# Optimization experiments

Measured on AMD Instinct MI355X. Metric: run time of the kernel, lower is better.

The kernel has to match this reference:

```python
import jax, jax.numpy as jnp
import numpy as np
from jax import lax

FEAT_STRIDE = 16
SCALES = np.array([8, 16, 32], dtype=np.float64)
RATIOS = np.array([0.5, 1, 2], dtype=np.float64)
PRE_NMS_TOP_N = 6000
POST_NMS_TOP_N = 1000
NMS_THRESH = 0.7

# ---- anchor generation (numpy, static constants) ----

def _whctrs(a):
    w = a[2] - a[0] + 1.0
    h = a[3] - a[1] + 1.0
    return w, h, a[0] + 0.5 * (w - 1.0), a[1] + 0.5 * (h - 1.0)

def _mkanchors(ws, hs, xc, yc):
    return np.stack([xc - 0.5 * (ws - 1.0), yc - 0.5 * (hs - 1.0),
                     xc + 0.5 * (ws - 1.0), yc + 0.5 * (hs - 1.0)], axis=1)

def _ratio_enum(anchor, ratios):
    w, h, xc, yc = _whctrs(anchor)
    size = w * h
    ws = np.round(np.sqrt(size / ratios))
    hs = np.round(ws * ratios)
    return _mkanchors(ws, hs, xc, yc)

def _scale_enum(anchor, scales):
    w, h, xc, yc = _whctrs(anchor)
    return _mkanchors(w * scales, h * scales, xc, yc)

def generate_anchors(base_size=16):
    base = np.array([1, 1, base_size, base_size], dtype=np.float64) - 1.0
    ra = _ratio_enum(base, RATIOS)
    return np.vstack([_scale_enum(ra[i], SCALES) for i in range(ra.shape[0])]).astype(np.float32)


def setup_inputs() -> dict:
    key = jax.random.key(0)
    k1, k2 = jax.random.split(key)
    H, W, A = 76, 128, 9
    scores = jax.random.uniform(k1, (1, 2 * A, H, W), dtype=jnp.float32)
    bbox_delta = jax.random.normal(k2, (1, 4 * A, H, W), dtype=jnp.float32) * 0.1
    im_info = jnp.array([H * FEAT_STRIDE, W * FEAT_STRIDE, 1.0], dtype=jnp.float32)  # [h, w, scale]
    return {"scores": scores, "bbox_delta": bbox_delta, "im_info": im_info}


def reference(scores, bbox_delta, im_info):
    anchors = generate_anchors()            # [A, 4]
    A = anchors.shape[0]
    H, W = scores.shape[2], scores.shape[3]

    # grid of shifted anchors: [K*A, 4], anchor index varies fastest (matches permute layout)
    sx = np.arange(W) * FEAT_STRIDE
    sy = np.arange(H) * FEAT_STRIDE
    sx, sy = np.meshgrid(sx, sy)
    shifts = np.stack([sx.ravel(), sy.ravel(), sx.ravel(), sy.ravel()], axis=1).astype(np.float32)  # [K,4]
    all_anchors = jnp.asarray((anchors[None, :, :] + shifts[:, None, :]).reshape(-1, 4))  # [K*A,4]

    # foreground scores, NHWC flatten -> [K*A]
    fg = jnp.transpose(scores[0, A:], (1, 2, 0)).reshape(-1)
    # deltas, NHWC flatten -> [K*A, 4]
    deltas = jnp.transpose(bbox_delta[0], (1, 2, 0)).reshape(-1, 4)

    aw = all_anchors[:, 2] - all_anchors[:, 0] + 1.0
    ah = all_anchors[:, 3] - all_anchors[:, 1] + 1.0
    acx = all_anchors[:, 0] + 0.5 * aw
    acy = all_anchors[:, 1] + 0.5 * ah
    pcx = deltas[:, 0] * aw + acx
    pcy = deltas[:, 1] * ah + acy
    pw = jnp.exp(deltas[:, 2]) * aw
    ph = jnp.exp(deltas[:, 3]) * ah
    boxes = jnp.stack([pcx - 0.5 * pw, pcy - 0.5 * ph, pcx + 0.5 * pw, pcy + 0.5 * ph], axis=1)

    # clip_boxes to image
    xmax = im_info[1] - 1.0
    ymax = im_info[0] - 1.0
    boxes = jnp.stack([jnp.clip(boxes[:, 0], 0.0, xmax), jnp.clip(boxes[:, 1], 0.0, ymax),
                       jnp.clip(boxes[:, 2], 0.0, xmax), jnp.clip(boxes[:, 3], 0.0, ymax)], axis=1)

    # pre-NMS top-N by fg score
    top_scores, top_idx = lax.top_k(fg, PRE_NMS_TOP_N)
    props = boxes[top_idx]                  # [N, 4], sorted by score desc

    # pairwise IoU (+1 convention)
    x1, y1, x2, y2 = props[:, 0], props[:, 1], props[:, 2], props[:, 3]
    areas = (x2 - x1 + 1.0) * (y2 - y1 + 1.0)
    iw = jnp.clip(jnp.minimum(x2[:, None], x2[None, :]) - jnp.maximum(x1[:, None], x1[None, :]) + 1.0, 0.0)
    ih = jnp.clip(jnp.minimum(y2[:, None], y2[None, :]) - jnp.maximum(y1[:, None], y1[None, :]) + 1.0, 0.0)
    inter = iw * ih
    iou = inter / (areas[:, None] + areas[None, :] - inter)  # [N, N]

    # sequential greedy NMS over score-sorted boxes
    N = PRE_NMS_TOP_N
    later = jnp.arange(N)
    def body(i, keep):
        sup = (iou[i] > NMS_THRESH) & keep[i] & (later > i)
        return keep & ~sup
    keep = lax.fori_loop(0, N, body, jnp.ones((N,), dtype=bool))

    masked = jnp.where(keep, top_scores, -jnp.inf)
    _, sel = lax.top_k(masked, POST_NMS_TOP_N)
    return props[sel]                       # [POST_NMS_TOP_N, 4]
```

## Files before the change

### kernel.cpp

```cpp
#include <hip/hip_runtime.h>
#include <cstdint>

#define HH 76
#define WW 128
#define AA 9
#define HWH (HH * WW)
#define KK (HWH * AA)
#define NSEL 6000
#define NCH 94
#define NPAD (NCH * 64)
#define NOUT 1000
#define NMS_T 0.7
#define NTRI (NCH * (NCH + 1) / 2)
#define MASK_BLOCKS 1117
#define SELCAP 16384
#define BINCAP 2048
#define HIST_BLOCKS 22
#define NBIN 16384

#define LBAR() asm volatile("s_waitcnt lgkmcnt(0)\n\ts_barrier" ::: "memory")

#define WS_HIST 0
#define WS_BINB 65536
#define WS_NACT 65540
#define WS_DONE1 65544
#define WS_ZERO_BYTES 65552
#define WS_ACTIVE 65552
#define WS_BINBASE 98320
#define WS_SELKEYS 163856
#define WS_BOXES 294928
#define WS_MASK 391184

__device__ __constant__ float c_ax1[9] = {-84.f, -176.f, -360.f, -56.f, -120.f, -248.f, -36.f, -80.f, -168.f};
__device__ __constant__ float c_ay1[9] = {-40.f, -88.f, -184.f, -56.f, -120.f, -248.f, -80.f, -168.f, -344.f};
__device__ __constant__ float c_ax2[9] = {99.f, 191.f, 375.f, 71.f, 135.f, 263.f, 51.f, 95.f, 183.f};
__device__ __constant__ float c_ay2[9] = {55.f, 103.f, 199.f, 71.f, 135.f, 263.f, 95.f, 183.f, 359.f};

__device__ __forceinline__ unsigned score_key(float s) {
    unsigned u = __float_as_uint(s);
    return (u & 0x80000000u) ? ~u : (u | 0x80000000u);
}

__device__ __forceinline__ int key_bin(unsigned key) {
    int bi = (int)(key >> 16) - 0x8000;
    return bi < 0 ? 0 : (bi > NBIN - 1 ? NBIN - 1 : bi);
}

__device__ __forceinline__ unsigned long long chunk_scan_fix(unsigned long long col,
                                                             unsigned long long alive_in) {
    unsigned long long kept = alive_in;
    while (true) {
        unsigned long long sup = __ballot((int)((col & kept) != 0ull));
        unsigned long long kept2 = alive_in & ~sup;
        if (kept2 == kept) return kept;
        kept = kept2;
    }
}

__global__ __launch_bounds__(1024) void k_histfind(const float* __restrict__ scores,
                                                   unsigned* __restrict__ histG,
                                                   unsigned* __restrict__ binB,
                                                   unsigned* __restrict__ binBase,
                                                   unsigned* __restrict__ activeList,
                                                   unsigned* __restrict__ nact,
                                                   unsigned* __restrict__ done) {
    __shared__ unsigned hloc[NBIN];
    int t = threadIdx.x;
#pragma unroll
    for (int k = 0; k < NBIN / 1024; ++k) hloc[t + k * 1024] = 0;
    __syncthreads();
    int gid = blockIdx.x * 1024 + t;
    if (gid < KK / 4) {
        float4 v = ((const float4*)(scores + AA * HWH))[gid];
        atomicAdd(&hloc[key_bin(score_key(v.x))], 1u);
        atomicAdd(&hloc[key_bin(score_key(v.y))], 1u);
        atomicAdd(&hloc[key_bin(score_key(v.z))], 1u);
        atomicAdd(&hloc[key_bin(score_key(v.w))], 1u);
    }
    __syncthreads();
#pragma unroll
    for (int k = 0; k < NBIN / 1024; ++k) {
        unsigned c = hloc[t + k * 1024];
        if (c) atomicAdd(&histG[t + k * 1024], c);
    }
    __threadfence();
    __shared__ unsigned lastS;
    if (t == 0) lastS = (atomicAdd(done, 1u) == (unsigned)gridDim.x - 1u) ? 1u : 0u;
    __syncthreads();
    if (!lastS) return;
    __threadfence();

    __shared__ unsigned seg[1024];
    __shared__ unsigned Bsh;
    unsigned local[16];
    unsigned ssum = 0;
#pragma unroll
    for (int k = 0; k < 16; ++k) { local[k] = histG[t * 16 + k]; ssum += local[k]; }
    seg[t] = ssum;
    __syncthreads();
    for (int off = 1; off < 1024; off <<= 1) {
        unsigned v = seg[t];
        unsigned add = (t + off < 1024) ? seg[t + off] : 0u;
        __syncthreads();
        seg[t] = v + add;
        __syncthreads();
    }
    unsigned above = (t + 1 < 1024) ? seg[t + 1] : 0u;
    if (above < NSEL && above + ssum >= NSEL) {
        unsigned acc = above;
#pragma unroll
        for (int b = 15; b >= 0; --b) {
            acc += local[b];
            if (acc >= NSEL) { Bsh = (unsigned)(t * 16 + b); *binB = Bsh; break; }
        }
    }
    __syncthreads();
    unsigned B = Bsh;
    if ((unsigned)(t * 16 + 15) >= B) {
        unsigned acc2 = above;
        for (int k = 15; k >= 0; --k) {
            unsigned bin = (unsigned)(t * 16 + k);
            if (bin < B) break;
            if (local[k] > 0) {
                binBase[bin] = acc2;
                unsigned tick = atomicAdd(nact, 1u);
                if (tick < 8192) activeList[tick] = bin;
            }
            acc2 += local[k];
        }
    }
}

__global__ __launch_bounds__(1024) void k_gather(const float* __restrict__ scores,
                                                 const unsigned* __restrict__ binB,
                                                 unsigned* __restrict__ binBase,
                                                 unsigned long long* __restrict__ selKeys) {
    int j4 = blockIdx.x * 1024 + threadIdx.x;
    if (j4 >= KK / 4) return;
    float4 v = ((const float4*)(scores + AA * HWH))[j4];
    unsigned B = *binB;
    float sv[4] = {v.x, v.y, v.z, v.w};
#pragma unroll
    for (int k = 0; k < 4; ++k) {
        int j = j4 * 4 + k;
        unsigned key = score_key(sv[k]);
        unsigned bin = (unsigned)key_bin(key);
        if (bin >= B) {
            int a = j / HWH;
            int hw = j - a * HWH;
            unsigned i = (unsigned)(hw * AA + a);
            unsigned pos = atomicAdd(&binBase[bin], 1u);
            if (pos < SELCAP)
                selKeys[pos] = ((unsigned long long)key << 32) | (unsigned)(~i);
        }
    }
}

__global__ __launch_bounds__(256) void k_binsort(const unsigned* __restrict__ histG,
                                                 const unsigned* __restrict__ binBase,
                                                 const unsigned* __restrict__ activeList,
                                                 const unsigned* __restrict__ nact,
                                                 unsigned long long* __restrict__ selKeys,
                                                 const float* __restrict__ bbox,
                                                 const float* __restrict__ im_info,
                                                 float4* __restrict__ boxes) {
    __shared__ unsigned long long sk[BINCAP];
    int t = threadIdx.x;
    unsigned na = *nact;
    if (na > 8192) na = 8192;
    double xmax = (double)im_info[1] - 1.0, ymax = (double)im_info[0] - 1.0;
    for (unsigned aIdx = blockIdx.x; aIdx < na; aIdx += gridDim.x) {
        unsigned bin = activeList[aIdx];
        unsigned ntot = histG[bin];
        unsigned base = binBase[bin] - ntot;
        unsigned n = ntot > BINCAP ? BINCAP : ntot;
        unsigned m = 64; while (m < n) m <<= 1;
        for (unsigned p = t; p < m; p += 256) sk[p] = (p < n) ? selKeys[base + p] : 0ull;
        __syncthreads();
        for (unsigned size = 2; size <= m; size <<= 1) {
            for (unsigned stride = size >> 1; stride > 0; stride >>= 1) {
                for (unsigned p = (unsigned)t; p < m / 2; p += 256) {
                    unsigned i = 2u * p - (p & (stride - 1u));
                    unsigned j = i + stride;
                    bool up = (i & size) != 0;
                    unsigned long long a = sk[i], b = sk[j];
                    bool doswap = up ? (a > b) : (a < b);
                    if (doswap) { sk[i] = b; sk[j] = a; }
                }
                __syncthreads();
            }
        }
        for (unsigned r = t; r < n; r += 256) {
            unsigned g = base + r;
            if (g >= NSEL) continue;
            unsigned i = ~(unsigned)(sk[r] & 0xFFFFFFFFull);
            int a = (int)(i % AA);
            int hw = (int)(i / AA);
            int h = hw >> 7, w = hw & 127;
            double sx = 16.0 * w, sy = 16.0 * h;
            double ax1 = (double)c_ax1[a] + sx, ay1 = (double)c_ay1[a] + sy;
            double ax2 = (double)c_ax2[a] + sx, ay2 = (double)c_ay2[a] + sy;
            double aw = ax2 - ax1 + 1.0, ah = ay2 - ay1 + 1.0;
            double acx = ax1 + 0.5 * aw, acy = ay1 + 0.5 * ah;
            int bse = h * WW + w;
            double d0 = (double)bbox[(4 * a + 0) * HWH + bse];
            double d1 = (double)bbox[(4 * a + 1) * HWH + bse];
            double d2 = (double)bbox[(4 * a + 2) * HWH + bse];
            double d3 = (double)bbox[(4 * a + 3) * HWH + bse];
            double pcx = d0 * aw + acx, pcy = d1 * ah + acy;
            double pw = exp(d2) * aw, ph = exp(d3) * ah;
            double x1 = fmin(fmax(pcx - 0.5 * pw, 0.0), xmax);
            double y1 = fmin(fmax(pcy - 0.5 * ph, 0.0), ymax);
            double x2 = fmin(fmax(pcx + 0.5 * pw, 0.0), xmax);
            double y2 = fmin(fmax(pcy + 0.5 * ph, 0.0), ymax);
            boxes[g] = make_float4((float)x1, (float)y1, (float)x2, (float)y2);
        }
        __syncthreads();
    }
}

__global__ __launch_bounds__(256) void k_mask(const float4* __restrict__ boxes,
                                              unsigned long long* __restrict__ supT) {
    __shared__ float4 cb[4][64];
    int wave = threadIdx.x >> 6, lane = threadIdx.x & 63;
    for (int L = blockIdx.x * 4 + wave; L < NTRI; L += MASK_BLOCKS * 4) {
        int rc = 0, rem = L;
        while (rem >= NCH - rc) { rem -= NCH - rc; rc++; }
        int cc = rc + rem;
        cb[wave][lane] = boxes[cc * 64 + lane];
        int gi = rc * 64 + lane;
        unsigned long long bits = 0ull;
        if (gi < NSEL) {
            float4 rb = boxes[gi];
            double rx1 = rb.x, ry1 = rb.y, rx2 = rb.z, ry2 = rb.w;
            double rarea = (rx2 - rx1 + 1.0) * (ry2 - ry1 + 1.0);
            for (int j = 0; j < 64; ++j) {
                int gj = cc * 64 + j;
                float4 c = cb[wave][j];
                double iw = fmin(rx2, (double)c.z) - fmax(rx1, (double)c.x) + 1.0;
                double ih = fmin(ry2, (double)c.w) - fmax(ry1, (double)c.y) + 1.0;
                if (gj > gi && gj < NSEL && iw > 0.0 && ih > 0.0) {
                    double inter = iw * ih;
                    double carea = ((double)c.z - (double)c.x + 1.0) * ((double)c.w - (double)c.y + 1.0);
                    double uni = rarea + carea - inter;
                    if (inter > NMS_T * uni) bits |= (1ull << j);
                }
            }
        }
        unsigned long long myword = 0ull;
        for (int j = 0; j < 64; ++j) {
            unsigned long long bal = __ballot((int)((bits >> j) & 1ull));
            if (lane == j) myword = bal;
        }
        supT[(size_t)rc * NPAD + cc * 64 + lane] = myword;
    }
}

__global__ __launch_bounds__(512, 1) void k_nms(const unsigned long long* __restrict__ supT,
                                                const float4* __restrict__ boxes,
                                                float4* __restrict__ out) {
    __shared__ unsigned long long colLds[NCH][64];
    __shared__ unsigned long long removed[NCH];
    __shared__ unsigned long long aliveArr[NCH];
    __shared__ int cstop;
    __shared__ unsigned scanBuf[8];
    int t = threadIdx.x;
    int wave = t >> 6, lane = t & 63;

    for (int c = wave; c < NCH; c += 8)
        colLds[c][lane] = supT[(size_t)c * NPAD + c * 64 + lane];
    for (int i = t; i < NCH; i += 512) removed[i] = (i == NCH - 1) ? 0xFFFF000000000000ull : 0ull;
    if (t == 0) cstop = -1;
    __syncthreads();
    if (wave == 0) __builtin_amdgcn_s_setprio(1);

    unsigned long long wAA = 0, wAB = 0;
    unsigned long long mA[8], mB[8];
#pragma unroll
    for (int q = 0; q < 8; ++q) { mA[q] = 0; mB[q] = 0; }
    if (wave == 0) wAA = supT[(size_t)0 * NPAD + 1 * 64 + lane];
    unsigned keptTot = 0;

    for (int c = 0; c < NCH; c += 2) {
        if (wave == 0) {
            if (c + 2 < NCH) wAB = supT[(size_t)(c + 1) * NPAD + (c + 2) * 64 + lane];
            unsigned long long alive_in = ~removed[c];
            unsigned long long alive = chunk_scan_fix(colLds[c][lane], alive_in);
            keptTot += (unsigned)__popcll(alive);
            if (lane == 0) {
                removed[c] = ~alive;
                aliveArr[c] = alive;
                if (keptTot >= NOUT) cstop = c;
            }
            if (c + 1 < NCH) {
                unsigned long long ball = __ballot((int)((wAA & alive) != 0ull));
                if (lane == 0 && ball) atomicOr(&removed[c + 1], ball);
            }
        } else {
            if (c + 2 < NCH) {
#pragma unroll
                for (int q = 0; q < 8; ++q) {
                    int cp = (wave - 1) + 7 * q;
                    mB[q] = (cp < c + 1) ? supT[(size_t)cp * NPAD + (c + 2) * 64 + lane] : 0ull;
                }
            }
            if (c + 1 < NCH) {
                unsigned long long acc = 0ull;
#pragma unroll
                for (int q = 0; q < 8; ++q) {
                    int cp = (wave - 1) + 7 * q;
                    if (cp < c) acc |= __ballot((int)((mA[q] & aliveArr[cp]) != 0ull));
                }
                for (int cp = (wave - 1) + 56; cp < c; cp += 7) {
                    unsigned long long wv = supT[(size_t)cp * NPAD + (c + 1) * 64 + lane];
                    acc |= __ballot((int)((wv & aliveArr[cp]) != 0ull));
                }
                if (lane == 0 && acc) atomicOr(&removed[c + 1], acc);
            }
        }
        LBAR();
        if (cstop >= 0) break;
        if (c + 1 >= NCH) break;

        if (wave == 0) {
            if (c + 3 < NCH) wAA = supT[(size_t)(c + 2) * NPAD + (c + 3) * 64 + lane];
            unsigned long long alive_in = ~removed[c + 1];
            unsigned long long alive = chunk_scan_fix(colLds[c + 1][lane], alive_in);
            keptTot += (unsigned)__popcll(alive);
            if (lane == 0) {
                removed[c + 1] = ~alive;
                aliveArr[c + 1] = alive;
                if (keptTot >= NOUT) cstop = c + 1;
            }
            if (c + 2 < NCH) {
                unsigned long long ball = __ballot((int)((wAB & alive) != 0ull));
                if (lane == 0 && ball) atomicOr(&removed[c + 2], ball);
            }
        } else {
            if (c + 3 < NCH) {
#pragma unroll
                for (int q = 0; q < 8; ++q) {
                    int cp = (wave - 1) + 7 * q;
                    mA[q] = (cp < c + 2) ? supT[(size_t)cp * NPAD + (c + 3) * 64 + lane] : 0ull;
                }
            }
            if (c + 2 < NCH) {
                unsigned long long acc = 0ull;
#pragma unroll
                for (int q = 0; q < 8; ++q) {
                    int cp = (wave - 1) + 7 * q;
                    if (cp < c + 1) acc |= __ballot((int)((mB[q] & aliveArr[cp]) != 0ull));
                }
                for (int cp = (wave - 1) + 56; cp < c + 1; cp += 7) {
                    unsigned long long wv = supT[(size_t)cp * NPAD + (c + 2) * 64 + lane];
                    acc |= __ballot((int)((wv & aliveArr[cp]) != 0ull));
                }
                if (lane == 0 && acc) atomicOr(&removed[c + 2], acc);
            }
        }
        LBAR();
        if (cstop >= 0) break;
    }
    if (wave == 0) __builtin_amdgcn_s_setprio(0);
    __syncthreads();

    int base = t * 12;
    unsigned cnt = 0, keepbits = 0;
    for (int q = 0; q < 12; ++q) {
        int i = base + q;
        if (i < NSEL) {
            bool kp = !((removed[i >> 6] >> (i & 63)) & 1ull);
            if (kp) { cnt++; keepbits |= (1u << q); }
        }
    }
    unsigned v = cnt;
#pragma unroll
    for (int off = 1; off < 64; off <<= 1) {
        unsigned u = (unsigned)__shfl_up((int)v, off, 64);
        if (lane >= off) v += u;
    }
    if (lane == 63) scanBuf[wave] = v;
    __syncthreads();
    unsigned waveOff = 0, NK = 0;
#pragma unroll
    for (int ww = 0; ww < 8; ++ww) {
        unsigned wv = scanBuf[ww];
        if (ww < wave) waveOff += wv;
        NK += wv;
    }
    unsigned incl = waveOff + v;
    unsigned kpos = incl - cnt;
    for (int q = 0; q < 12; ++q) {
        int i = base + q;
        if (i < NSEL) {
            bool kp = (keepbits >> q) & 1u;
            unsigned pos = kp ? kpos : (NK + (unsigned)i - kpos);
            if (kp) kpos++;
            if (pos < NOUT) out[pos] = boxes[i];
        }
    }
}

extern "C" void kernel_launch(void* const* d_in, const int* in_sizes, int n_in,
                              void* d_out, int out_size, void* d_ws, size_t ws_size,
                              hipStream_t stream) {
    const float* scores = (const float*)d_in[0];
    const float* bbox = (const float*)d_in[1];
    const float* im_info = (const float*)d_in[2];
    char* ws = (char*)d_ws;

    unsigned* histG = (unsigned*)(ws + WS_HIST);
    unsigned* binB = (unsigned*)(ws + WS_BINB);
    unsigned* nact = (unsigned*)(ws + WS_NACT);
    unsigned* done1 = (unsigned*)(ws + WS_DONE1);
    unsigned* activeList = (unsigned*)(ws + WS_ACTIVE);
    unsigned* binBase = (unsigned*)(ws + WS_BINBASE);
    unsigned long long* selKeys = (unsigned long long*)(ws + WS_SELKEYS);
    float4* boxes = (float4*)(ws + WS_BOXES);
    unsigned long long* supT = (unsigned long long*)(ws + WS_MASK);
    float4* out = (float4*)d_out;

    hipMemsetAsync(ws, 0, WS_ZERO_BYTES, stream);

    k_histfind<<<HIST_BLOCKS, 1024, 0, stream>>>(scores, histG, binB, binBase, activeList, nact, done1);
    k_gather<<<HIST_BLOCKS, 1024, 0, stream>>>(scores, binB, binBase, selKeys);
    k_binsort<<<64, 256, 0, stream>>>(histG, binBase, activeList, nact, selKeys, bbox, im_info, boxes);
    k_mask<<<MASK_BLOCKS, 256, 0, stream>>>(boxes, supT);
    k_nms<<<1, 512, 0, stream>>>(supT, boxes, out);
}
```

Before: 115.6 us.

## Fold histogram into single-block kernel and drop workspace memset

Replaces the 22-block histogram kernel, which merged partial histograms through global atomics and a last-block-done counter, with a single 1024-thread block that builds the full histogram in shared memory and finds the threshold bin directly. This removes the hipMemsetAsync launch, the global histogram atomics and the cross-block completion handshake. Only the active bins' counts are written to global memory for later kernels. In exchange, all 87K score reads and shared-memory atomics now run on one compute unit. That serialises the scan across the chip and may lengthen this stage.

```diff
diff --git a/kernel.cpp b/kernel.cpp
--- a/kernel.cpp
+++ b/kernel.cpp
@@ -15,7 +15,7 @@
 #define MASK_BLOCKS 1117
 #define SELCAP 16384
 #define BINCAP 2048
-#define HIST_BLOCKS 22
+#define GATHER_BLOCKS 22
 #define NBIN 16384
 
 #define LBAR() asm volatile("s_waitcnt lgkmcnt(0)\n\ts_barrier" ::: "memory")
@@ -23,8 +23,6 @@
 #define WS_HIST 0
 #define WS_BINB 65536
 #define WS_NACT 65540
-#define WS_DONE1 65544
-#define WS_ZERO_BYTES 65552
 #define WS_ACTIVE 65552
 #define WS_BINBASE 98320
 #define WS_SELKEYS 163856
@@ -57,45 +55,33 @@
     }
 }
 
-__global__ __launch_bounds__(1024) void k_histfind(const float* __restrict__ scores,
-                                                   unsigned* __restrict__ histG,
-                                                   unsigned* __restrict__ binB,
-                                                   unsigned* __restrict__ binBase,
-                                                   unsigned* __restrict__ activeList,
-                                                   unsigned* __restrict__ nact,
-                                                   unsigned* __restrict__ done) {
+__global__ __launch_bounds__(1024) void k_front1(const float* __restrict__ scores,
+                                                 unsigned* __restrict__ histG,
+                                                 unsigned* __restrict__ binB,
+                                                 unsigned* __restrict__ binBase,
+                                                 unsigned* __restrict__ activeList,
+                                                 unsigned* __restrict__ nact) {
     __shared__ unsigned hloc[NBIN];
+    __shared__ unsigned seg[1024];
+    __shared__ unsigned Bsh;
     int t = threadIdx.x;
+    if (t == 0) *nact = 0;
 #pragma unroll
     for (int k = 0; k < NBIN / 1024; ++k) hloc[t + k * 1024] = 0;
     __syncthreads();
-    int gid = blockIdx.x * 1024 + t;
-    if (gid < KK / 4) {
-        float4 v = ((const float4*)(scores + AA * HWH))[gid];
+    for (int g = t; g < KK / 4; g += 1024) {
+        float4 v = ((const float4*)(scores + AA * HWH))[g];
         atomicAdd(&hloc[key_bin(score_key(v.x))], 1u);
         atomicAdd(&hloc[key_bin(score_key(v.y))], 1u);
         atomicAdd(&hloc[key_bin(score_key(v.z))], 1u);
         atomicAdd(&hloc[key_bin(score_key(v.w))], 1u);
     }
     __syncthreads();
-#pragma unroll
-    for (int k = 0; k < NBIN / 1024; ++k) {
-        unsigned c = hloc[t + k * 1024];
-        if (c) atomicAdd(&histG[t + k * 1024], c);
-    }
-    __threadfence();
-    __shared__ unsigned lastS;
-    if (t == 0) lastS = (atomicAdd(done, 1u) == (unsigned)gridDim.x - 1u) ? 1u : 0u;
-    __syncthreads();
-    if (!lastS) return;
-    __threadfence();
-
-    __shared__ unsigned seg[1024];
-    __shared__ unsigned Bsh;
+
     unsigned local[16];
     unsigned ssum = 0;
 #pragma unroll
-    for (int k = 0; k < 16; ++k) { local[k] = histG[t * 16 + k]; ssum += local[k]; }
+    for (int k = 0; k < 16; ++k) { local[k] = hloc[t * 16 + k]; ssum += local[k]; }
     seg[t] = ssum;
     __syncthreads();
     for (int off = 1; off < 1024; off <<= 1) {
@@ -123,6 +109,7 @@
             if (bin < B) break;
             if (local[k] > 0) {
                 binBase[bin] = acc2;
+                histG[bin] = local[k];
                 unsigned tick = atomicAdd(nact, 1u);
                 if (tick < 8192) activeList[tick] = bin;
             }
@@ -412,7 +399,6 @@
     unsigned* histG = (unsigned*)(ws + WS_HIST);
     unsigned* binB = (unsigned*)(ws + WS_BINB);
     unsigned* nact = (unsigned*)(ws + WS_NACT);
-    unsigned* done1 = (unsigned*)(ws + WS_DONE1);
     unsigned* activeList = (unsigned*)(ws + WS_ACTIVE);
     unsigned* binBase = (unsigned*)(ws + WS_BINBASE);
     unsigned long long* selKeys = (unsigned long long*)(ws + WS_SELKEYS);
@@ -420,10 +406,8 @@
     unsigned long long* supT = (unsigned long long*)(ws + WS_MASK);
     float4* out = (float4*)d_out;
 
-    hipMemsetAsync(ws, 0, WS_ZERO_BYTES, stream);
-
-    k_histfind<<<HIST_BLOCKS, 1024, 0, stream>>>(scores, histG, binB, binBase, activeList, nact, done1);
-    k_gather<<<HIST_BLOCKS, 1024, 0, stream>>>(scores, binB, binBase, selKeys);
+    k_front1<<<1, 1024, 0, stream>>>(scores, histG, binB, binBase, activeList, nact);
+    k_gather<<<GATHER_BLOCKS, 1024, 0, stream>>>(scores, binB, binBase, selKeys);
     k_binsort<<<64, 256, 0, stream>>>(histG, binBase, activeList, nact, selKeys, bbox, im_info, boxes);
     k_mask<<<MASK_BLOCKS, 256, 0, stream>>>(boxes, supT);
     k_nms<<<1, 512, 0, stream>>>(supT, boxes, out);
```

After: 108.3 us. 6.4% less time.
